# Optimization experiments

Measured on AMD Instinct MI355X. Metric: run time of the kernel, lower is better.

## Reference

```python
import jax, jax.numpy as jnp
import numpy as np

N, E, D_IN, H1, C1, D_OUT = 50000, 800000, 384, 4, 64, 5
D_HID = H1 * C1  # 256, input to layer 2


def setup_inputs() -> dict:
    key = jax.random.key(0)
    ks = jax.random.split(key, 12)

    def lin(k, i, o):
        return (jax.random.normal(k, (i, o), jnp.float32) / np.sqrt(i)).astype(jnp.float32)

    inp = {
        "x": jax.random.normal(ks[0], (N, D_IN), jnp.float32),
        "edge_index": jax.random.randint(ks[1], (2, E), 0, N, jnp.int32),
        # layer 1: TransformerConv(384 -> 64, heads=4, concat=True)
        "Wq1": lin(ks[2], D_IN, H1 * C1), "bq1": jnp.zeros((H1 * C1,), jnp.float32),
        "Wk1": lin(ks[3], D_IN, H1 * C1), "bk1": jnp.zeros((H1 * C1,), jnp.float32),
        "Wv1": lin(ks[4], D_IN, H1 * C1), "bv1": jnp.zeros((H1 * C1,), jnp.float32),
        "Ws1": lin(ks[5], D_IN, H1 * C1), "bs1": jnp.zeros((H1 * C1,), jnp.float32),
        # layer 2: TransformerConv(256 -> 5, heads=1, concat=False)
        "Wq2": lin(ks[6], D_HID, D_OUT), "bq2": jnp.zeros((D_OUT,), jnp.float32),
        "Wk2": lin(ks[7], D_HID, D_OUT), "bk2": jnp.zeros((D_OUT,), jnp.float32),
        "Wv2": lin(ks[8], D_HID, D_OUT), "bv2": jnp.zeros((D_OUT,), jnp.float32),
        "Ws2": lin(ks[9], D_HID, D_OUT), "bs2": jnp.zeros((D_OUT,), jnp.float32),
    }
    return inp


def _segment_softmax(logits, dst, n):
    # logits: [E, H] grouped by destination node
    m = jax.ops.segment_max(logits, dst, num_segments=n)
    m = jnp.where(jnp.isfinite(m), m, 0.0)
    e = jnp.exp(logits - m[dst])
    s = jax.ops.segment_sum(e, dst, num_segments=n)
    return e / (s[dst] + 1e-16)


def _transformer_conv(x, src, dst, Wq, bq, Wk, bk, Wv, bv, Ws, bs, heads, out_ch, concat):
    n = x.shape[0]
    q = (x @ Wq + bq).reshape(n, heads, out_ch)
    k = (x @ Wk + bk).reshape(n, heads, out_ch)
    v = (x @ Wv + bv).reshape(n, heads, out_ch)
    # per-edge attention logits: q_i . k_j / sqrt(C)   [E, H]
    logits = jnp.einsum('ehc,ehc->eh', q[dst], k[src]) / jnp.sqrt(jnp.float32(out_ch))
    alpha = _segment_softmax(logits, dst, n)          # [E, H]
    msg = v[src] * alpha[:, :, None]                  # [E, H, C]
    out = jax.ops.segment_sum(msg, dst, num_segments=n)  # [N, H, C]
    out = out.reshape(n, heads * out_ch) if concat else out.mean(axis=1)
    # root skip connection (root_weight=True default in PyG)
    return out + (x @ Ws + bs)


def reference(x, edge_index, Wq1, bq1, Wk1, bk1, Wv1, bv1, Ws1, bs1,
              Wq2, bq2, Wk2, bk2, Wv2, bv2, Ws2, bs2):
    src, dst = edge_index[0], edge_index[1]
    h = _transformer_conv(x, src, dst, Wq1, bq1, Wk1, bk1, Wv1, bv1, Ws1, bs1,
                          H1, C1, True)
    h = jax.nn.relu(h)
    out = _transformer_conv(h, src, dst, Wq2, bq2, Wk2, bk2, Wv2, bv2, Ws2, bs2,
                            1, D_OUT, False)
    return out
```

## Files before the change

### kernel.cpp

```cpp
#include <hip/hip_runtime.h>
#include <hip/hip_bf16.h>

#define N_NODES 50000
#define N_EDGES 800000
#define NPAD    50048
#define SCAN_B  196

typedef __attribute__((ext_vector_type(8))) short bf16x8;
typedef __attribute__((ext_vector_type(8))) unsigned short u16x8;
typedef __attribute__((ext_vector_type(4))) float f32x4;

__device__ __forceinline__ unsigned short f2bf(float f) {
  union { float f; unsigned u; } x; x.f = f;
  unsigned r = x.u + 0x7fffu + ((x.u >> 16) & 1u);
  return (unsigned short)(r >> 16);
}
__device__ __forceinline__ float bf2f(unsigned short u) {
  union { unsigned u; float f; } x; x.u = ((unsigned)u) << 16;
  return x.f;
}
__device__ __forceinline__ unsigned char enc8(float v) {
  float t = fminf(fmaxf(fmaf(v, 16.f, 128.5f), 0.f), 255.f);
  return (unsigned char)(int)t;
}

__device__ __forceinline__ void gload16(const unsigned short* g, unsigned short* l) {
  __builtin_amdgcn_global_load_lds(
      (const __attribute__((address_space(1))) unsigned int*)g,
      (__attribute__((address_space(3))) unsigned int*)l, 16, 0, 0);
}

__global__ void hist_kernel(const int* __restrict__ dst, int* __restrict__ counts, int E) {
  int e = blockIdx.x * 256 + threadIdx.x;
  if (e < E) atomicAdd(&counts[dst[e]], 1);
}

__global__ __launch_bounds__(256) void scan1_kernel(const int* __restrict__ counts,
                                                    int* __restrict__ tmp, int* __restrict__ bsum, int n) {
  __shared__ int sm[256];
  int i = blockIdx.x * 256 + threadIdx.x;
  int v = (i < n) ? counts[i] : 0;
  sm[threadIdx.x] = v;
  __syncthreads();
  for (int off = 1; off < 256; off <<= 1) {
    int t = (threadIdx.x >= off) ? sm[threadIdx.x - off] : 0;
    __syncthreads();
    sm[threadIdx.x] += t;
    __syncthreads();
  }
  if (i < n) tmp[i] = sm[threadIdx.x] - v;
  if (threadIdx.x == 255) bsum[blockIdx.x] = sm[255];
}

__global__ __launch_bounds__(256) void scan2_kernel(const int* __restrict__ bsum,
                                                    int* __restrict__ bbase, int nb) {
  __shared__ int sm[256];
  int v = (threadIdx.x < nb) ? bsum[threadIdx.x] : 0;
  sm[threadIdx.x] = v;
  __syncthreads();
  for (int off = 1; off < 256; off <<= 1) {
    int t = (threadIdx.x >= off) ? sm[threadIdx.x - off] : 0;
    __syncthreads();
    sm[threadIdx.x] += t;
    __syncthreads();
  }
  if (threadIdx.x < nb) bbase[threadIdx.x] = sm[threadIdx.x] - v;
}

__global__ __launch_bounds__(256) void scan3_kernel(const int* __restrict__ tmp,
                                                    const int* __restrict__ bbase,
                                                    int* __restrict__ offsets, int* __restrict__ cursor,
                                                    int n, int E) {
  int i = blockIdx.x * 256 + threadIdx.x;
  if (i < n) {
    int o = tmp[i] + bbase[blockIdx.x];
    offsets[i] = o;
    cursor[i] = o;
  }
  if (i == 0) offsets[n] = E;
}

__global__ void scatter_kernel(const int* __restrict__ src, const int* __restrict__ dst,
                               int* __restrict__ cursor, int* __restrict__ csr_src, int E) {
  int e = blockIdx.x * 256 + threadIdx.x;
  if (e < E) {
    int pos = atomicAdd(&cursor[dst[e]], 1);
    csr_src[pos] = src[e];
  }
}

__global__ void convert_x_kernel(const float* __restrict__ x, unsigned short* __restrict__ xb,
                                 int total_real, int total_pad) {
  long i = ((long)blockIdx.x * 256 + threadIdx.x) * 8;
  if (i >= total_pad) return;
  u16x8 o;
  if (i < total_real) {
    float4 v0 = *(const float4*)&x[i];
    float4 v1 = *(const float4*)&x[i + 4];
    o[0] = (short)f2bf(v0.x); o[1] = (short)f2bf(v0.y);
    o[2] = (short)f2bf(v0.z); o[3] = (short)f2bf(v0.w);
    o[4] = (short)f2bf(v1.x); o[5] = (short)f2bf(v1.y);
    o[6] = (short)f2bf(v1.z); o[7] = (short)f2bf(v1.w);
  } else {
    o = (u16x8)0;
  }
  *(u16x8*)&xb[i] = o;
}

__global__ void pack_w1_kernel(const float* __restrict__ Wq, const float* __restrict__ Wk,
                               const float* __restrict__ Wv, const float* __restrict__ Ws,
                               const float* __restrict__ bq, const float* __restrict__ bk,
                               const float* __restrict__ bv, const float* __restrict__ bs_,
                               unsigned short* __restrict__ wbt, float* __restrict__ bias1) {
  int idx = blockIdx.x * 256 + threadIdx.x;
  if (idx >= 1024 * 384) return;
  int n = idx / 384, k = idx - n * 384;
  int blk = n >> 8, cc = n & 255;
  const float* W = (blk == 0) ? Wq : (blk == 1) ? Wk : (blk == 2) ? Wv : Ws;
  wbt[idx] = f2bf(W[(long)k * 256 + cc]);
  if (k == 0) {
    const float* b = (blk == 0) ? bq : (blk == 1) ? bk : (blk == 2) ? bv : bs_;
    bias1[n] = b[cc];
  }
}

__global__ void pack_w2_kernel(const float* __restrict__ Wq, const float* __restrict__ Wk,
                               const float* __restrict__ Wv, const float* __restrict__ Ws,
                               const float* __restrict__ bq, const float* __restrict__ bk,
                               const float* __restrict__ bv, const float* __restrict__ bs_,
                               unsigned short* __restrict__ w2bt, float* __restrict__ bias2) {
  int idx = blockIdx.x * 256 + threadIdx.x;
  if (idx >= 32 * 256) return;
  int c = idx >> 8, p = idx & 255;
  unsigned short o = 0;
  if (c < 20) {
    int blk = c / 5, cc = c - blk * 5;
    int tch = (p & 0xC0) + (p & 3) * 16 + ((p & 63) >> 2);
    const float* W = (blk == 0) ? Wq : (blk == 1) ? Wk : (blk == 2) ? Wv : Ws;
    o = f2bf(W[(long)tch * 5 + cc]);
    if (p == 0) {
      const float* b = (blk == 0) ? bq : (blk == 1) ? bk : (blk == 2) ? bv : bs_;
      bias2[c] = b[cc];
    }
  }
  w2bt[idx] = o;
}

__global__ __launch_bounds__(512) void gemm1_kernel(
    const unsigned short* __restrict__ xb, const unsigned short* __restrict__ wbt,
    const float* __restrict__ bias,
    unsigned short* __restrict__ qb, unsigned char* __restrict__ kvb,
    unsigned short* __restrict__ s1b) {
  __shared__ unsigned short As[128 * 32];
  __shared__ unsigned short Bs[256 * 32];
  int tid = threadIdx.x;
  long m0 = (long)blockIdx.x * 128;
  int n0 = blockIdx.y * 256;
  int w = tid >> 6, l = tid & 63;
  int wr = (w >> 2) * 64, wc = (w & 3) * 64;
  int lr = l & 15, c0 = l >> 4;
  int sw = (lr ^ (lr >> 2)) & 3;
  int swoff = (c0 ^ sw) * 8;
  f32x4 acc[4][4] = {};
  int rs = tid >> 2, ss = tid & 3;
  int fa = (rs ^ (rs >> 2)) & 3;
  int fb1 = ((rs + 128) ^ ((rs + 128) >> 2)) & 3;
  const unsigned short* gA  = xb + (m0 + rs) * 384 + ((ss ^ fa) * 8);
  const unsigned short* gB0 = wbt + (long)(n0 + rs) * 384 + ((ss ^ fa) * 8);
  const unsigned short* gB1 = wbt + (long)(n0 + rs + 128) * 384 + ((ss ^ fb1) * 8);
  for (int kt = 0; kt < 12; ++kt) {
    int ko = kt * 32;
    __syncthreads();
    gload16(gA + ko, &As[tid * 8]);
    gload16(gB0 + ko, &Bs[tid * 8]);
    gload16(gB1 + ko, &Bs[4096 + tid * 8]);
    __syncthreads();
    bf16x8 af[4], bfv[4];
#pragma unroll
    for (int mf = 0; mf < 4; ++mf) af[mf] = *(const bf16x8*)&As[(wr + mf * 16 + lr) * 32 + swoff];
#pragma unroll
    for (int nf = 0; nf < 4; ++nf) bfv[nf] = *(const bf16x8*)&Bs[(wc + nf * 16 + lr) * 32 + swoff];
#pragma unroll
    for (int mf = 0; mf < 4; ++mf)
#pragma unroll
      for (int nf = 0; nf < 4; ++nf)
        acc[mf][nf] = __builtin_amdgcn_mfma_f32_16x16x32_bf16(af[mf], bfv[nf], acc[mf][nf], 0, 0, 0);
  }
  int y = blockIdx.y;
  float bv[4];
#pragma unroll
  for (int nf = 0; nf < 4; ++nf) bv[nf] = bias[n0 + wc + nf * 16 + lr];
  int pos = wc + lr * 4;
#pragma unroll
  for (int mf = 0; mf < 4; ++mf) {
#pragma unroll
    for (int i = 0; i < 4; ++i) {
      long row = m0 + wr + mf * 16 + c0 * 4 + i;
      float v0 = acc[mf][0][i] + bv[0];
      float v1 = acc[mf][1][i] + bv[1];
      float v2 = acc[mf][2][i] + bv[2];
      float v3 = acc[mf][3][i] + bv[3];
      if (y == 0 || y == 3) {
        ushort4 st;
        st.x = f2bf(v0); st.y = f2bf(v1); st.z = f2bf(v2); st.w = f2bf(v3);
        unsigned short* dst = (y == 0) ? qb : s1b;
        *(ushort4*)&dst[row * 256 + pos] = st;
      } else {
        uchar4 st;
        st.x = enc8(v0); st.y = enc8(v1); st.z = enc8(v2); st.w = enc8(v3);
        *(uchar4*)&kvb[row * 512 + ((y == 1) ? 0 : 256) + pos] = st;
      }
    }
  }
}

__global__ __launch_bounds__(256) void agg1_kernel(
    const unsigned short* __restrict__ qb, const unsigned char* __restrict__ kvb,
    unsigned short* s1b,
    const int* __restrict__ offsets, const int* __restrict__ csr_src) {
  int w = threadIdx.x >> 6, l = threadIdx.x & 63;
  int n = blockIdx.x * 4 + w;
  if (n >= N_NODES) return;
  int g = l >> 4;
  int sub = l & 15;
  float qf[16];
  float qs = 0.f;
  {
    const unsigned short* qrow = qb + (long)n * 256 + sub * 16;
    u16x8 q0 = *(const u16x8*)qrow;
    u16x8 q1 = *(const u16x8*)(qrow + 8);
#pragma unroll
    for (int j = 0; j < 8; ++j) {
      qf[j] = bf2f((unsigned short)q0[j]) * 0.0078125f;
      qf[8 + j] = bf2f((unsigned short)q1[j]) * 0.0078125f;
    }
#pragma unroll
    for (int j = 0; j < 16; ++j) qs += qf[j];
    qs += __shfl_xor(qs, 1); qs += __shfl_xor(qs, 2);
  }
  float pc = 128.f * qs;
  float acc[16] = {};
  float se = 0.f;
  int i0 = offsets[n], i1 = offsets[n + 1];
#define DOT4(P, W, B) \
  P = fmaf(qf[(B) + 0], (float)((W) & 0xffu), P); \
  P = fmaf(qf[(B) + 1], (float)(((W) >> 8) & 0xffu), P); \
  P = fmaf(qf[(B) + 2], (float)(((W) >> 16) & 0xffu), P); \
  P = fmaf(qf[(B) + 3], (float)((W) >> 24), P);
#define VACC(E, W, B) \
  acc[(B) + 0] = fmaf(E, (float)((W) & 0xffu), acc[(B) + 0]); \
  acc[(B) + 1] = fmaf(E, (float)(((W) >> 8) & 0xffu), acc[(B) + 1]); \
  acc[(B) + 2] = fmaf(E, (float)(((W) >> 16) & 0xffu), acc[(B) + 2]); \
  acc[(B) + 3] = fmaf(E, (float)((W) >> 24), acc[(B) + 3]);
  for (int i = i0; i < i1; i += 8) {
    int ia = i + g, ib = i + 4 + g;
    int sa = csr_src[ia < i1 ? ia : i1 - 1];
    int sb = csr_src[ib < i1 ? ib : i1 - 1];
    const uint4* pa = (const uint4*)(kvb + (long)sa * 512 + sub * 16);
    const uint4* pb = (const uint4*)(kvb + (long)sb * 512 + sub * 16);
    uint4 ka = pa[0], va = pa[16];
    uint4 kw = pb[0], vw = pb[16];
    float pa_ = 0.f, pb_ = 0.f;
    DOT4(pa_, ka.x, 0) DOT4(pa_, ka.y, 4) DOT4(pa_, ka.z, 8) DOT4(pa_, ka.w, 12)
    DOT4(pb_, kw.x, 0) DOT4(pb_, kw.y, 4) DOT4(pb_, kw.z, 8) DOT4(pb_, kw.w, 12)
    pa_ += __shfl_xor(pa_, 1); pa_ += __shfl_xor(pa_, 2);
    pb_ += __shfl_xor(pb_, 1); pb_ += __shfl_xor(pb_, 2);
    float ea = (ia < i1) ? __expf(pa_ - pc) : 0.f;
    float eb = (ib < i1) ? __expf(pb_ - pc) : 0.f;
    se += ea + eb;
    VACC(ea, va.x, 0) VACC(ea, va.y, 4) VACC(ea, va.z, 8) VACC(ea, va.w, 12)
    VACC(eb, vw.x, 0) VACC(eb, vw.y, 4) VACC(eb, vw.z, 8) VACC(eb, vw.w, 12)
  }
#undef DOT4
#undef VACC
#pragma unroll
  for (int j = 0; j < 16; ++j) {
    acc[j] += __shfl_xor(acc[j], 16);
    acc[j] += __shfl_xor(acc[j], 32);
  }
  se += __shfl_xor(se, 16);
  se += __shfl_xor(se, 32);
  if (g == 0) {
    float inv = (se > 0.f) ? 1.0f / se : 0.f;
    float bias = (se > 0.f) ? -8.0f : 0.f;
    long ob = (long)n * 256 + sub * 16;
    u16x8 sv0 = *(const u16x8*)&s1b[ob];
    u16x8 sv1 = *(const u16x8*)&s1b[ob + 8];
    u16x8 h0, h1;
#pragma unroll
    for (int j = 0; j < 8; ++j) {
      float v0 = fmaf(acc[j] * inv, 0.0625f, bias);
      float v1 = fmaf(acc[8 + j] * inv, 0.0625f, bias);
      h0[j] = (short)f2bf(fmaxf(v0 + bf2f((unsigned short)sv0[j]), 0.f));
      h1[j] = (short)f2bf(fmaxf(v1 + bf2f((unsigned short)sv1[j]), 0.f));
    }
    *(u16x8*)&s1b[ob] = h0;
    *(u16x8*)&s1b[ob + 8] = h1;
  }
}

__global__ __launch_bounds__(256) void lin2_kernel(const unsigned short* __restrict__ hb,
                                                   const unsigned short* __restrict__ w2bt,
                                                   const float* __restrict__ bias2,
                                                   float* __restrict__ qs2, float* __restrict__ kv2) {
  __shared__ unsigned short Bs2[32 * 264];
  __shared__ float bsh[32];
  for (int i = threadIdx.x; i < 32 * 32; i += 256) {
    int r = i >> 5, cc = i & 31;
    *(u16x8*)&Bs2[r * 264 + cc * 8] = *(const u16x8*)&w2bt[r * 256 + cc * 8];
  }
  if (threadIdx.x < 32) bsh[threadIdx.x] = (threadIdx.x < 20) ? bias2[threadIdx.x] : 0.f;
  __syncthreads();
  int w = threadIdx.x >> 6, l = threadIdx.x & 63;
  long row0 = (long)blockIdx.x * 128 + w * 32;
  int lr = l & 15, c0 = l >> 4;
  f32x4 acc[2][2] = {};
  for (int kk = 0; kk < 8; ++kk) {
    int koff = kk * 32 + c0 * 8;
    bf16x8 af[2], bfv[2];
    af[0] = *(const bf16x8*)&hb[(row0 + lr) * 256 + koff];
    af[1] = *(const bf16x8*)&hb[(row0 + 16 + lr) * 256 + koff];
    bfv[0] = *(const bf16x8*)&Bs2[lr * 264 + koff];
    bfv[1] = *(const bf16x8*)&Bs2[(16 + lr) * 264 + koff];
#pragma unroll
    for (int mf = 0; mf < 2; ++mf)
#pragma unroll
      for (int nf = 0; nf < 2; ++nf)
        acc[mf][nf] = __builtin_amdgcn_mfma_f32_16x16x32_bf16(af[mf], bfv[nf], acc[mf][nf], 0, 0, 0);
  }
#pragma unroll
  for (int mf = 0; mf < 2; ++mf) {
#pragma unroll
    for (int nf = 0; nf < 2; ++nf) {
      int col = nf * 16 + lr;
#pragma unroll
      for (int i = 0; i < 4; ++i) {
        long n = row0 + mf * 16 + c0 * 4 + i;
        float v = acc[mf][nf][i] + bsh[col];
        if (col < 5) qs2[n * 12 + col] = v;
        else if (col < 15) kv2[n * 12 + (col - 5)] = v;
        else if (col < 20) qs2[n * 12 + (col - 10)] = v;
      }
    }
  }
}

__global__ void agg2_kernel(const float* __restrict__ qs2, const float* __restrict__ kv2,
                            const int* __restrict__ offsets, const int* __restrict__ csr_src,
                            float* __restrict__ out) {
  int n = blockIdx.x * 256 + threadIdx.x;
  if (n >= N_NODES) return;
  const float* bn = &qs2[(long)n * 12];
  const float is5 = 0.4472135954999579f;
  float q[5], acc[5] = {0, 0, 0, 0, 0}, se = 0.f;
#pragma unroll
  for (int c = 0; c < 5; ++c) q[c] = bn[c] * is5;
  int i0 = offsets[n], i1 = offsets[n + 1];
  for (int i = i0; i < i1; ++i) {
    int s = csr_src[i];
    const float4* ps = (const float4*)&kv2[(long)s * 12];
    float4 A = ps[0], B = ps[1], C = ps[2];
    float lg = q[0] * A.x + q[1] * A.y + q[2] * A.z + q[3] * A.w + q[4] * B.x;
    float ee = __expf(lg);
    se += ee;
    acc[0] += ee * B.y; acc[1] += ee * B.z; acc[2] += ee * B.w;
    acc[3] += ee * C.x; acc[4] += ee * C.y;
  }
  float inv = 1.f / (se + 1e-16f);
#pragma unroll
  for (int c = 0; c < 5; ++c) out[(long)n * 5 + c] = acc[c] * inv + bn[5 + c];
}

extern "C" void kernel_launch(void* const* d_in, const int* in_sizes, int n_in,
                              void* d_out, int out_size, void* d_ws, size_t ws_size,
                              hipStream_t stream) {
  (void)in_sizes; (void)n_in; (void)out_size; (void)ws_size;
  const float* x   = (const float*)d_in[0];
  const int* eidx  = (const int*)d_in[1];
  const int* esrc  = eidx;
  const int* edst  = eidx + N_EDGES;
  const float* Wq1 = (const float*)d_in[2];  const float* bq1 = (const float*)d_in[3];
  const float* Wk1 = (const float*)d_in[4];  const float* bk1 = (const float*)d_in[5];
  const float* Wv1 = (const float*)d_in[6];  const float* bv1 = (const float*)d_in[7];
  const float* Ws1 = (const float*)d_in[8];  const float* bs1 = (const float*)d_in[9];
  const float* Wq2 = (const float*)d_in[10]; const float* bq2 = (const float*)d_in[11];
  const float* Wk2 = (const float*)d_in[12]; const float* bk2 = (const float*)d_in[13];
  const float* Wv2 = (const float*)d_in[14]; const float* bv2 = (const float*)d_in[15];
  const float* Ws2 = (const float*)d_in[16]; const float* bs2 = (const float*)d_in[17];

  char* p = (char*)d_ws;
  auto take = [&](size_t bytes) { char* r = p; p += (bytes + 255) & ~(size_t)255; return r; };
  unsigned short* xb  = (unsigned short*)take((size_t)NPAD * 384 * 2);
  unsigned short* wbt = (unsigned short*)take((size_t)1024 * 384 * 2);
  float* bias1        = (float*)take(1024 * 4);
  unsigned short* qb  = (unsigned short*)take((size_t)NPAD * 256 * 2);
  unsigned char* kvb  = (unsigned char*)take((size_t)NPAD * 512);
  unsigned short* s1b = (unsigned short*)take((size_t)NPAD * 256 * 2);
  unsigned short* w2bt = (unsigned short*)take(32 * 256 * 2);
  float* bias2        = (float*)take(32 * 4);
  float* qs2          = (float*)take((size_t)NPAD * 12 * 4);
  float* kv2          = (float*)take((size_t)NPAD * 12 * 4);
  int* counts         = (int*)take((size_t)N_NODES * 4);
  int* offsets        = (int*)take((size_t)(N_NODES + 1) * 4);
  int* cursor         = (int*)take((size_t)N_NODES * 4);
  int* csr_src        = (int*)take((size_t)N_EDGES * 4);
  int* scan_tmp       = (int*)take((size_t)N_NODES * 4);
  int* scan_bsum      = (int*)take(256 * 4);
  int* scan_bbase     = (int*)take(256 * 4);

  hipMemsetAsync(counts, 0, (size_t)N_NODES * 4, stream);
  hist_kernel<<<(N_EDGES + 255) / 256, 256, 0, stream>>>(edst, counts, N_EDGES);
  scan1_kernel<<<SCAN_B, 256, 0, stream>>>(counts, scan_tmp, scan_bsum, N_NODES);
  scan2_kernel<<<1, 256, 0, stream>>>(scan_bsum, scan_bbase, SCAN_B);
  scan3_kernel<<<SCAN_B, 256, 0, stream>>>(scan_tmp, scan_bbase, offsets, cursor, N_NODES, N_EDGES);
  scatter_kernel<<<(N_EDGES + 255) / 256, 256, 0, stream>>>(esrc, edst, cursor, csr_src, N_EDGES);
  convert_x_kernel<<<(NPAD * 384 / 8 + 255) / 256, 256, 0, stream>>>(x, xb, N_NODES * 384, NPAD * 384);
  pack_w1_kernel<<<(1024 * 384 + 255) / 256, 256, 0, stream>>>(Wq1, Wk1, Wv1, Ws1, bq1, bk1, bv1, bs1, wbt, bias1);
  pack_w2_kernel<<<(32 * 256 + 255) / 256, 256, 0, stream>>>(Wq2, Wk2, Wv2, Ws2, bq2, bk2, bv2, bs2, w2bt, bias2);
  gemm1_kernel<<<dim3(NPAD / 128, 4), 512, 0, stream>>>(xb, wbt, bias1, qb, kvb, s1b);
  agg1_kernel<<<(N_NODES + 3) / 4, 256, 0, stream>>>(qb, kvb, s1b, offsets, csr_src);
  lin2_kernel<<<NPAD / 128, 256, 0, stream>>>(s1b, w2bt, bias2, qs2, kv2);
  agg2_kernel<<<(N_NODES + 255) / 256, 256, 0, stream>>>(qs2, kv2, offsets, csr_src, (float*)d_out);
}
```

Before: 279.7 us.

## Quantize Q/K to int8 with sdot4, double-buffer GEMM LDS, persistent agg grid

Q and K are now stored as signed int8 and the attention logit is computed with packed int8 dot products (sdot4) in place of float unpack-and-FMA. This removes the per-node softmax offset and halves Q storage. The layer-1 GEMM gains double-buffered LDS tiles so the next K-slice load overlaps the MFMA work, and its blocks are remapped into groups so the four output column tiles of a row block run close together. The aggregation kernel becomes a grid-stride loop over a fixed 2048 blocks. The extra quantization of Q and K adds precision risk, and the logits are no longer max-shifted.

```diff
diff --git a/kernel.cpp b/kernel.cpp
--- a/kernel.cpp
+++ b/kernel.cpp
@@ -19,9 +19,30 @@
   union { unsigned u; float f; } x; x.u = ((unsigned)u) << 16;
   return x.f;
 }
-__device__ __forceinline__ unsigned char enc8(float v) {
+__device__ __forceinline__ unsigned char enc8v(float v) {
   float t = fminf(fmaxf(fmaf(v, 16.f, 128.5f), 0.f), 255.f);
   return (unsigned char)(int)t;
+}
+__device__ __forceinline__ char enc8k(float v) {
+  float t = fminf(fmaxf(v * 16.f, -127.f), 127.f);
+  return (char)(int)floorf(t + 0.5f);
+}
+__device__ __forceinline__ char enc8q(float v) {
+  float t = fminf(fmaxf(v * 24.f, -127.f), 127.f);
+  return (char)(int)floorf(t + 0.5f);
+}
+
+__device__ __forceinline__ int dot4i8(int a, int b, int c) {
+#if __has_builtin(__builtin_amdgcn_sdot4)
+  return __builtin_amdgcn_sdot4(a, b, c, false);
+#else
+  int r = c;
+  r += (int)(char)(a) * (int)(char)(b);
+  r += (int)(char)(a >> 8) * (int)(char)(b >> 8);
+  r += (int)(char)(a >> 16) * (int)(char)(b >> 16);
+  r += (int)(char)(a >> 24) * (int)(char)(b >> 24);
+  return r;
+#endif
 }
 
 __device__ __forceinline__ void gload16(const unsigned short* g, unsigned short* l) {
@@ -149,13 +170,18 @@
 __global__ __launch_bounds__(512) void gemm1_kernel(
     const unsigned short* __restrict__ xb, const unsigned short* __restrict__ wbt,
     const float* __restrict__ bias,
-    unsigned short* __restrict__ qb, unsigned char* __restrict__ kvb,
+    char* __restrict__ qb8, unsigned char* __restrict__ kvb,
     unsigned short* __restrict__ s1b) {
-  __shared__ unsigned short As[128 * 32];
-  __shared__ unsigned short Bs[256 * 32];
+  __shared__ unsigned short As[2][128 * 32];
+  __shared__ unsigned short Bs[2][256 * 32];
+  int bid = blockIdx.x;
+  int grp = bid >> 5, bl = bid & 31;
+  int mx = grp * 8 + (bl & 7);
+  int y = bl >> 3;
+  if (mx >= NPAD / 128) return;
   int tid = threadIdx.x;
-  long m0 = (long)blockIdx.x * 128;
-  int n0 = blockIdx.y * 256;
+  long m0 = (long)mx * 128;
+  int n0 = y * 256;
   int w = tid >> 6, l = tid & 63;
   int wr = (w >> 2) * 64, wc = (w & 3) * 64;
   int lr = l & 15, c0 = l >> 4;
@@ -168,25 +194,30 @@
   const unsigned short* gA  = xb + (m0 + rs) * 384 + ((ss ^ fa) * 8);
   const unsigned short* gB0 = wbt + (long)(n0 + rs) * 384 + ((ss ^ fa) * 8);
   const unsigned short* gB1 = wbt + (long)(n0 + rs + 128) * 384 + ((ss ^ fb1) * 8);
+  gload16(gA, &As[0][tid * 8]);
+  gload16(gB0, &Bs[0][tid * 8]);
+  gload16(gB1, &Bs[0][4096 + tid * 8]);
+  __syncthreads();
   for (int kt = 0; kt < 12; ++kt) {
-    int ko = kt * 32;
-    __syncthreads();
-    gload16(gA + ko, &As[tid * 8]);
-    gload16(gB0 + ko, &Bs[tid * 8]);
-    gload16(gB1 + ko, &Bs[4096 + tid * 8]);
-    __syncthreads();
+    int b = kt & 1;
+    if (kt < 11) {
+      int ko = (kt + 1) * 32;
+      gload16(gA + ko, &As[b ^ 1][tid * 8]);
+      gload16(gB0 + ko, &Bs[b ^ 1][tid * 8]);
+      gload16(gB1 + ko, &Bs[b ^ 1][4096 + tid * 8]);
+    }
     bf16x8 af[4], bfv[4];
 #pragma unroll
-    for (int mf = 0; mf < 4; ++mf) af[mf] = *(const bf16x8*)&As[(wr + mf * 16 + lr) * 32 + swoff];
-#pragma unroll
-    for (int nf = 0; nf < 4; ++nf) bfv[nf] = *(const bf16x8*)&Bs[(wc + nf * 16 + lr) * 32 + swoff];
+    for (int mf = 0; mf < 4; ++mf) af[mf] = *(const bf16x8*)&As[b][(wr + mf * 16 + lr) * 32 + swoff];
+#pragma unroll
+    for (int nf = 0; nf < 4; ++nf) bfv[nf] = *(const bf16x8*)&Bs[b][(wc + nf * 16 + lr) * 32 + swoff];
 #pragma unroll
     for (int mf = 0; mf < 4; ++mf)
 #pragma unroll
       for (int nf = 0; nf < 4; ++nf)
         acc[mf][nf] = __builtin_amdgcn_mfma_f32_16x16x32_bf16(af[mf], bfv[nf], acc[mf][nf], 0, 0, 0);
-  }
-  int y = blockIdx.y;
+    __syncthreads();
+  }
   float bv[4];
 #pragma unroll
   for (int nf = 0; nf < 4; ++nf) bv[nf] = bias[n0 + wc + nf * 16 + lr];
@@ -200,102 +231,88 @@
       float v1 = acc[mf][1][i] + bv[1];
       float v2 = acc[mf][2][i] + bv[2];
       float v3 = acc[mf][3][i] + bv[3];
-      if (y == 0 || y == 3) {
-        ushort4 st;
-        st.x = f2bf(v0); st.y = f2bf(v1); st.z = f2bf(v2); st.w = f2bf(v3);
-        unsigned short* dst = (y == 0) ? qb : s1b;
-        *(ushort4*)&dst[row * 256 + pos] = st;
+      if (y == 0) {
+        char4 st; st.x = enc8q(v0); st.y = enc8q(v1); st.z = enc8q(v2); st.w = enc8q(v3);
+        *(char4*)&qb8[row * 256 + pos] = st;
+      } else if (y == 1) {
+        char4 st; st.x = enc8k(v0); st.y = enc8k(v1); st.z = enc8k(v2); st.w = enc8k(v3);
+        *(char4*)&kvb[row * 512 + pos] = st;
+      } else if (y == 2) {
+        uchar4 st; st.x = enc8v(v0); st.y = enc8v(v1); st.z = enc8v(v2); st.w = enc8v(v3);
+        *(uchar4*)&kvb[row * 512 + 256 + pos] = st;
       } else {
-        uchar4 st;
-        st.x = enc8(v0); st.y = enc8(v1); st.z = enc8(v2); st.w = enc8(v3);
-        *(uchar4*)&kvb[row * 512 + ((y == 1) ? 0 : 256) + pos] = st;
+        ushort4 st; st.x = f2bf(v0); st.y = f2bf(v1); st.z = f2bf(v2); st.w = f2bf(v3);
+        *(ushort4*)&s1b[row * 256 + pos] = st;
       }
     }
   }
 }
 
 __global__ __launch_bounds__(256) void agg1_kernel(
-    const unsigned short* __restrict__ qb, const unsigned char* __restrict__ kvb,
+    const char* __restrict__ qb8, const unsigned char* __restrict__ kvb,
     unsigned short* s1b,
     const int* __restrict__ offsets, const int* __restrict__ csr_src) {
   int w = threadIdx.x >> 6, l = threadIdx.x & 63;
-  int n = blockIdx.x * 4 + w;
-  if (n >= N_NODES) return;
   int g = l >> 4;
   int sub = l & 15;
-  float qf[16];
-  float qs = 0.f;
-  {
-    const unsigned short* qrow = qb + (long)n * 256 + sub * 16;
-    u16x8 q0 = *(const u16x8*)qrow;
-    u16x8 q1 = *(const u16x8*)(qrow + 8);
-#pragma unroll
-    for (int j = 0; j < 8; ++j) {
-      qf[j] = bf2f((unsigned short)q0[j]) * 0.0078125f;
-      qf[8 + j] = bf2f((unsigned short)q1[j]) * 0.0078125f;
-    }
-#pragma unroll
-    for (int j = 0; j < 16; ++j) qs += qf[j];
-    qs += __shfl_xor(qs, 1); qs += __shfl_xor(qs, 2);
-  }
-  float pc = 128.f * qs;
-  float acc[16] = {};
-  float se = 0.f;
-  int i0 = offsets[n], i1 = offsets[n + 1];
-#define DOT4(P, W, B) \
-  P = fmaf(qf[(B) + 0], (float)((W) & 0xffu), P); \
-  P = fmaf(qf[(B) + 1], (float)(((W) >> 8) & 0xffu), P); \
-  P = fmaf(qf[(B) + 2], (float)(((W) >> 16) & 0xffu), P); \
-  P = fmaf(qf[(B) + 3], (float)((W) >> 24), P);
+  for (int n = blockIdx.x * 4 + w; n < N_NODES; n += gridDim.x * 4) {
+    int4 qi = *(const int4*)&qb8[(long)n * 256 + sub * 16];
+    float acc[16] = {};
+    float se = 0.f;
+    int i0 = offsets[n], i1 = offsets[n + 1];
 #define VACC(E, W, B) \
-  acc[(B) + 0] = fmaf(E, (float)((W) & 0xffu), acc[(B) + 0]); \
-  acc[(B) + 1] = fmaf(E, (float)(((W) >> 8) & 0xffu), acc[(B) + 1]); \
-  acc[(B) + 2] = fmaf(E, (float)(((W) >> 16) & 0xffu), acc[(B) + 2]); \
-  acc[(B) + 3] = fmaf(E, (float)((W) >> 24), acc[(B) + 3]);
-  for (int i = i0; i < i1; i += 8) {
-    int ia = i + g, ib = i + 4 + g;
-    int sa = csr_src[ia < i1 ? ia : i1 - 1];
-    int sb = csr_src[ib < i1 ? ib : i1 - 1];
-    const uint4* pa = (const uint4*)(kvb + (long)sa * 512 + sub * 16);
-    const uint4* pb = (const uint4*)(kvb + (long)sb * 512 + sub * 16);
-    uint4 ka = pa[0], va = pa[16];
-    uint4 kw = pb[0], vw = pb[16];
-    float pa_ = 0.f, pb_ = 0.f;
-    DOT4(pa_, ka.x, 0) DOT4(pa_, ka.y, 4) DOT4(pa_, ka.z, 8) DOT4(pa_, ka.w, 12)
-    DOT4(pb_, kw.x, 0) DOT4(pb_, kw.y, 4) DOT4(pb_, kw.z, 8) DOT4(pb_, kw.w, 12)
-    pa_ += __shfl_xor(pa_, 1); pa_ += __shfl_xor(pa_, 2);
-    pb_ += __shfl_xor(pb_, 1); pb_ += __shfl_xor(pb_, 2);
-    float ea = (ia < i1) ? __expf(pa_ - pc) : 0.f;
-    float eb = (ib < i1) ? __expf(pb_ - pc) : 0.f;
-    se += ea + eb;
-    VACC(ea, va.x, 0) VACC(ea, va.y, 4) VACC(ea, va.z, 8) VACC(ea, va.w, 12)
-    VACC(eb, vw.x, 0) VACC(eb, vw.y, 4) VACC(eb, vw.z, 8) VACC(eb, vw.w, 12)
-  }
-#undef DOT4
+    acc[(B) + 0] = fmaf(E, (float)((W) & 0xffu), acc[(B) + 0]); \
+    acc[(B) + 1] = fmaf(E, (float)(((W) >> 8) & 0xffu), acc[(B) + 1]); \
+    acc[(B) + 2] = fmaf(E, (float)(((W) >> 16) & 0xffu), acc[(B) + 2]); \
+    acc[(B) + 3] = fmaf(E, (float)((W) >> 24), acc[(B) + 3]);
+    for (int i = i0; i < i1; i += 8) {
+      int ia = i + g, ib = i + 4 + g;
+      int sa = csr_src[ia < i1 ? ia : i1 - 1];
+      int sb = csr_src[ib < i1 ? ib : i1 - 1];
+      const char* ba = (const char*)kvb + (long)sa * 512 + sub * 16;
+      const char* bb = (const char*)kvb + (long)sb * 512 + sub * 16;
+      int4 ka = *(const int4*)ba;
+      int4 kw = *(const int4*)bb;
+      uint4 va = *(const uint4*)(ba + 256);
+      uint4 vw = *(const uint4*)(bb + 256);
+      int da = 0, db = 0;
+      da = dot4i8(qi.x, ka.x, da); da = dot4i8(qi.y, ka.y, da);
+      da = dot4i8(qi.z, ka.z, da); da = dot4i8(qi.w, ka.w, da);
+      db = dot4i8(qi.x, kw.x, db); db = dot4i8(qi.y, kw.y, db);
+      db = dot4i8(qi.z, kw.z, db); db = dot4i8(qi.w, kw.w, db);
+      da += __shfl_xor(da, 1); da += __shfl_xor(da, 2);
+      db += __shfl_xor(db, 1); db += __shfl_xor(db, 2);
+      float ea = (ia < i1) ? __expf((float)da * (1.f / 3072.f)) : 0.f;
+      float eb = (ib < i1) ? __expf((float)db * (1.f / 3072.f)) : 0.f;
+      se += ea + eb;
+      VACC(ea, va.x, 0) VACC(ea, va.y, 4) VACC(ea, va.z, 8) VACC(ea, va.w, 12)
+      VACC(eb, vw.x, 0) VACC(eb, vw.y, 4) VACC(eb, vw.z, 8) VACC(eb, vw.w, 12)
+    }
 #undef VACC
 #pragma unroll
-  for (int j = 0; j < 16; ++j) {
-    acc[j] += __shfl_xor(acc[j], 16);
-    acc[j] += __shfl_xor(acc[j], 32);
-  }
-  se += __shfl_xor(se, 16);
-  se += __shfl_xor(se, 32);
-  if (g == 0) {
-    float inv = (se > 0.f) ? 1.0f / se : 0.f;
-    float bias = (se > 0.f) ? -8.0f : 0.f;
-    long ob = (long)n * 256 + sub * 16;
-    u16x8 sv0 = *(const u16x8*)&s1b[ob];
-    u16x8 sv1 = *(const u16x8*)&s1b[ob + 8];
-    u16x8 h0, h1;
-#pragma unroll
-    for (int j = 0; j < 8; ++j) {
-      float v0 = fmaf(acc[j] * inv, 0.0625f, bias);
-      float v1 = fmaf(acc[8 + j] * inv, 0.0625f, bias);
-      h0[j] = (short)f2bf(fmaxf(v0 + bf2f((unsigned short)sv0[j]), 0.f));
-      h1[j] = (short)f2bf(fmaxf(v1 + bf2f((unsigned short)sv1[j]), 0.f));
-    }
-    *(u16x8*)&s1b[ob] = h0;
-    *(u16x8*)&s1b[ob + 8] = h1;
+    for (int j = 0; j < 16; ++j) {
+      acc[j] += __shfl_xor(acc[j], 16);
+      acc[j] += __shfl_xor(acc[j], 32);
+    }
+    se += __shfl_xor(se, 16);
+    se += __shfl_xor(se, 32);
+    if (g == 0) {
+      float inv = (se > 0.f) ? 1.0f / se : 0.f;
+      float bias = (se > 0.f) ? -8.0f : 0.f;
+      long ob = (long)n * 256 + sub * 16;
+      u16x8 sv0 = *(const u16x8*)&s1b[ob];
+      u16x8 sv1 = *(const u16x8*)&s1b[ob + 8];
+      u16x8 h0, h1;
+#pragma unroll
+      for (int j = 0; j < 8; ++j) {
+        float v0 = fmaf(acc[j] * inv, 0.0625f, bias);
+        float v1 = fmaf(acc[8 + j] * inv, 0.0625f, bias);
+        h0[j] = (short)f2bf(fmaxf(v0 + bf2f((unsigned short)sv0[j]), 0.f));
+        h1[j] = (short)f2bf(fmaxf(v1 + bf2f((unsigned short)sv1[j]), 0.f));
+      }
+      *(u16x8*)&s1b[ob] = h0;
+      *(u16x8*)&s1b[ob + 8] = h1;
+    }
   }
 }
 
@@ -393,7 +410,7 @@
   unsigned short* xb  = (unsigned short*)take((size_t)NPAD * 384 * 2);
   unsigned short* wbt = (unsigned short*)take((size_t)1024 * 384 * 2);
   float* bias1        = (float*)take(1024 * 4);
-  unsigned short* qb  = (unsigned short*)take((size_t)NPAD * 256 * 2);
+  char* qb8           = (char*)take((size_t)NPAD * 256);
   unsigned char* kvb  = (unsigned char*)take((size_t)NPAD * 512);
   unsigned short* s1b = (unsigned short*)take((size_t)NPAD * 256 * 2);
   unsigned short* w2bt = (unsigned short*)take(32 * 256 * 2);
@@ -417,8 +434,8 @@
   convert_x_kernel<<<(NPAD * 384 / 8 + 255) / 256, 256, 0, stream>>>(x, xb, N_NODES * 384, NPAD * 384);
   pack_w1_kernel<<<(1024 * 384 + 255) / 256, 256, 0, stream>>>(Wq1, Wk1, Wv1, Ws1, bq1, bk1, bv1, bs1, wbt, bias1);
   pack_w2_kernel<<<(32 * 256 + 255) / 256, 256, 0, stream>>>(Wq2, Wk2, Wv2, Ws2, bq2, bk2, bv2, bs2, w2bt, bias2);
-  gemm1_kernel<<<dim3(NPAD / 128, 4), 512, 0, stream>>>(xb, wbt, bias1, qb, kvb, s1b);
-  agg1_kernel<<<(N_NODES + 3) / 4, 256, 0, stream>>>(qb, kvb, s1b, offsets, csr_src);
+  gemm1_kernel<<<((NPAD / 128 + 7) / 8) * 32, 512, 0, stream>>>(xb, wbt, bias1, qb8, kvb, s1b);
+  agg1_kernel<<<2048, 256, 0, stream>>>(qb8, kvb, s1b, offsets, csr_src);
   lin2_kernel<<<NPAD / 128, 256, 0, stream>>>(s1b, w2bt, bias2, qs2, kv2);
   agg2_kernel<<<(N_NODES + 255) / 256, 256, 0, stream>>>(qs2, kv2, offsets, csr_src, (float*)d_out);
 }
```

Result: no change. 279.7 us (-0.0%).
